# Kernel optimization log

Measured on AMD Instinct MI355X. Metric: run time of the kernel, lower is better.

## Reference

```python
import jax, jax.numpy as jnp
import numpy as np

D_MODEL = 1024
NUM_HEADS = 8
HEAD_DIM = D_MODEL // NUM_HEADS  # 128


def setup_inputs() -> dict:
    key = jax.random.key(0)
    ks = jax.random.split(key, 11)
    B, S = 2, 2048
    inp = {
        "query": jax.random.normal(ks[0], (B, S, D_MODEL), dtype=jnp.float32),
        "key": jax.random.normal(ks[1], (B, S, D_MODEL), dtype=jnp.float32),
        "value": jax.random.normal(ks[2], (B, S, D_MODEL), dtype=jnp.float32),
        # Dense layer params (Keras Dense: y = x @ W + b), glorot-ish scale
        "Wq": jax.random.normal(ks[3], (D_MODEL, D_MODEL), dtype=jnp.float32) * (1.0 / np.sqrt(D_MODEL)),
        "bq": jnp.zeros((D_MODEL,), dtype=jnp.float32),
        "Wk": jax.random.normal(ks[4], (D_MODEL, D_MODEL), dtype=jnp.float32) * (1.0 / np.sqrt(D_MODEL)),
        "bk": jnp.zeros((D_MODEL,), dtype=jnp.float32),
        "Wv": jax.random.normal(ks[5], (D_MODEL, D_MODEL), dtype=jnp.float32) * (1.0 / np.sqrt(D_MODEL)),
        "bv": jnp.zeros((D_MODEL,), dtype=jnp.float32),
        "Wo": jax.random.normal(ks[6], (D_MODEL, D_MODEL), dtype=jnp.float32) * (1.0 / np.sqrt(D_MODEL)),
        "bo": jnp.zeros((D_MODEL,), dtype=jnp.float32),
    }
    return inp


def _split_heads(x, B):
    # [B, S, D] -> [B, H, S, Hd]
    S = x.shape[1]
    return x.reshape(B, S, NUM_HEADS, HEAD_DIM).transpose(0, 2, 1, 3)


def reference(query, key, value, Wq, bq, Wk, bk, Wv, bv, Wo, bo):
    B, S, _ = query.shape
    q = _split_heads(query @ Wq + bq, B)   # [B,H,S,Hd]
    k = _split_heads(key @ Wk + bk, B)
    v = _split_heads(value @ Wv + bv, B)
    # ReLU (non-softmax) attention; scale by sqrt(per-head dk)
    scale = 1.0 / jnp.sqrt(jnp.float32(HEAD_DIM))
    score = jnp.einsum("bhqd,bhkd->bhqk", q, k) * scale  # [B,H,S,S]
    attn_weights = jax.nn.relu(score)
    # dropout inactive at inference (training=None)
    context = jnp.einsum("bhqk,bhkd->bhqd", attn_weights, v)  # [B,H,S,Hd]
    context = context.transpose(0, 2, 1, 3).reshape(B, S, D_MODEL)
    output = context @ Wo + bo
    return (output, attn_weights)
```

## Files before the change

### kernel.cpp

```cpp
#include <hip/hip_runtime.h>
#include <hip/hip_bf16.h>
#include <stdint.h>

#define D_MODEL 1024
#define NHEAD 8
#define HDIM 128
#define BATCH 2
#define SEQ 2048
#define MTOT (BATCH*SEQ)
#define KVBLK 64
#define NT (SEQ/KVBLK)

typedef __attribute__((ext_vector_type(4))) float f32x4;
typedef __attribute__((ext_vector_type(8))) short bf16x8;

__device__ __forceinline__ uint32_t swz128(uint32_t row, uint32_t cb) {
  return row * 128u + (cb ^ ((row & 7u) << 4));
}
__device__ __forceinline__ uint32_t swz256(uint32_t row, uint32_t cb) {
  return row * 256u + (cb ^ ((row & 7u) << 4));
}

__device__ __forceinline__ void gload16(void* lds, const void* g) {
  __builtin_amdgcn_global_load_lds(
      reinterpret_cast<const __attribute__((address_space(1))) uint32_t*>(
          reinterpret_cast<uintptr_t>(g)),
      reinterpret_cast<__attribute__((address_space(3))) uint32_t*>(
          (uint32_t)reinterpret_cast<uintptr_t>(lds)),
      16, 0, 0);
}

__global__ __launch_bounds__(256) void cast3(const float* __restrict__ q,
                                             const float* __restrict__ k,
                                             const float* __restrict__ v,
                                             __hip_bfloat16* __restrict__ out) {
  const float* src = blockIdx.y == 0 ? q : (blockIdx.y == 1 ? k : v);
  const size_t NE = (size_t)MTOT * D_MODEL;
  size_t i = ((size_t)blockIdx.x * 256 + threadIdx.x) * 8;
  float4 a = *reinterpret_cast<const float4*>(src + i);
  float4 b = *reinterpret_cast<const float4*>(src + i + 4);
  __hip_bfloat16 o[8] = {__float2bfloat16(a.x), __float2bfloat16(a.y),
                         __float2bfloat16(a.z), __float2bfloat16(a.w),
                         __float2bfloat16(b.x), __float2bfloat16(b.y),
                         __float2bfloat16(b.z), __float2bfloat16(b.w)};
  *reinterpret_cast<uint4*>(out + blockIdx.y * NE + i) =
      *reinterpret_cast<const uint4*>(o);
}

__global__ __launch_bounds__(256)
void transpose4(const float* __restrict__ s0, const float* __restrict__ s1,
                const float* __restrict__ s2, const float* __restrict__ s3,
                __hip_bfloat16* __restrict__ d0, __hip_bfloat16* __restrict__ d1,
                __hip_bfloat16* __restrict__ d2, __hip_bfloat16* __restrict__ d3) {
  const float* W = blockIdx.z == 0 ? s0 : blockIdx.z == 1 ? s1 : blockIdx.z == 2 ? s2 : s3;
  __hip_bfloat16* Wt = blockIdx.z == 0 ? d0 : blockIdx.z == 1 ? d1 : blockIdx.z == 2 ? d2 : d3;
  __shared__ float t[32][33];
  const int x = threadIdx.x, y = threadIdx.y;
  const int n0 = blockIdx.x * 32, k0 = blockIdx.y * 32;
#pragma unroll
  for (int i = 0; i < 4; ++i)
    t[y + i * 8][x] = W[(size_t)(k0 + y + i * 8) * D_MODEL + n0 + x];
  __syncthreads();
#pragma unroll
  for (int i = 0; i < 4; ++i)
    Wt[(size_t)(n0 + y + i * 8) * D_MODEL + k0 + x] = __float2bfloat16(t[x][y + i * 8]);
}

struct GemmArgs {
  const __hip_bfloat16* A;
  const __hip_bfloat16* B;
  const float* bias;
  void* out;
  int mode;
};

__global__ __launch_bounds__(256)
void gemm_gl(GemmArgs g0, GemmArgs g1, GemmArgs g2, int K) {
  __shared__ char ldsA[128 * 128];
  __shared__ char ldsB[128 * 128];
  GemmArgs ga = blockIdx.z == 0 ? g0 : (blockIdx.z == 1 ? g1 : g2);

  const int tid = threadIdx.x, lane = tid & 63, wid = tid >> 6;
  const int lrow = lane & 15, lko = (lane >> 4) * 8, rbase = (lane >> 4) * 4;
  const int m0 = blockIdx.x * 128, n0 = blockIdx.y * 128;
  const size_t ldb = (size_t)K * 2;

  const int srow = lane >> 3;
  const int sca = ((lane & 7) * 16) ^ (srow << 4);
  const char* Ab = (const char*)ga.A + (size_t)(m0 + wid * 32 + srow) * ldb + sca;
  const char* Bb = (const char*)ga.B + (size_t)(n0 + wid * 32 + srow) * ldb + sca;
  char* lA = ldsA + wid * 32 * 128;
  char* lB = ldsB + wid * 32 * 128;

  f32x4 acc[4][4];
  const f32x4 fz = {0.f, 0.f, 0.f, 0.f};
#pragma unroll
  for (int m = 0; m < 4; ++m)
#pragma unroll
    for (int n = 0; n < 4; ++n) acc[m][n] = fz;

  const int wm = (wid >> 1) * 64, wn = (wid & 1) * 64;

  for (int kt = 0; kt < K; kt += 64) {
    __syncthreads();
#pragma unroll
    for (int i = 0; i < 4; ++i) {
      gload16(lA + i * 8 * 128, Ab + (size_t)i * 8 * ldb + kt * 2);
      gload16(lB + i * 8 * 128, Bb + (size_t)i * 8 * ldb + kt * 2);
    }
    __syncthreads();
#pragma unroll
    for (int kk = 0; kk < 64; kk += 32) {
      bf16x8 af[4], bf[4];
#pragma unroll
      for (int m = 0; m < 4; ++m)
        af[m] = *reinterpret_cast<const bf16x8*>(&ldsA[swz128(wm + m * 16 + lrow, (kk + lko) * 2)]);
#pragma unroll
      for (int n = 0; n < 4; ++n)
        bf[n] = *reinterpret_cast<const bf16x8*>(&ldsB[swz128(wn + n * 16 + lrow, (kk + lko) * 2)]);
#pragma unroll
      for (int m = 0; m < 4; ++m)
#pragma unroll
        for (int n = 0; n < 4; ++n)
          acc[m][n] = __builtin_amdgcn_mfma_f32_16x16x32_bf16(af[m], bf[n], acc[m][n], 0, 0, 0);
    }
  }

  if (ga.mode == 2) {
#pragma unroll
    for (int m = 0; m < 4; ++m)
#pragma unroll
      for (int n = 0; n < 4; ++n) {
        const int col = n0 + wn + n * 16 + lrow;
        const float bv = ga.bias[col];
#pragma unroll
        for (int r = 0; r < 4; ++r) {
          const int row = m0 + wm + m * 16 + rbase + r;
          reinterpret_cast<float*>(ga.out)[(size_t)row * D_MODEL + col] = acc[m][n][r] + bv;
        }
      }
  } else if (ga.mode == 0) {
#pragma unroll
    for (int m = 0; m < 4; ++m)
#pragma unroll
      for (int n = 0; n < 4; ++n) {
        const int col = n0 + wn + n * 16 + lrow;
        const float bv = ga.bias[col];
        const int h = col >> 7, hd = col & 127;
#pragma unroll
        for (int r = 0; r < 4; ++r) {
          const int row = m0 + wm + m * 16 + rbase + r;
          const int b = row >> 11, s = row & 2047;
          reinterpret_cast<__hip_bfloat16*>(ga.out)[((size_t)(b * NHEAD + h) * SEQ + s) * HDIM + hd] =
              __float2bfloat16(acc[m][n][r] + bv);
        }
      }
  } else {
#pragma unroll
    for (int m = 0; m < 4; ++m)
#pragma unroll
      for (int n = 0; n < 4; ++n) {
        const int col = n0 + wn + n * 16 + lrow;
        const float bv = ga.bias[col];
        const int h = col >> 7, hd = col & 127;
#pragma unroll
        for (int r = 0; r < 4; ++r) {
          const int row = m0 + wm + m * 16 + rbase + r;
          const int b = row >> 11, s = row & 2047;
          reinterpret_cast<__hip_bfloat16*>(ga.out)[((size_t)(b * NHEAD + h) * HDIM + hd) * SEQ + s] =
              __float2bfloat16(acc[m][n][r] + bv);
        }
      }
  }
}

__global__ __launch_bounds__(512)
void attn_v2(const __hip_bfloat16* __restrict__ Qh,
             const __hip_bfloat16* __restrict__ Kh,
             const __hip_bfloat16* __restrict__ Vt,
             float* __restrict__ attn,
             __hip_bfloat16* __restrict__ ctx) {
  __shared__ char ldsK[2][KVBLK * 256];
  __shared__ char ldsV[2][HDIM * 128];
  __shared__ char ldsP[128 * 128];

  const int tid = threadIdx.x, lane = tid & 63, wid = tid >> 6;
  const int lrow = lane & 15, lko = (lane >> 4) * 8, rbase = (lane >> 4) * 4;
  const int wqq = (wid >> 1) * 32;
  const int wqk = (wid & 1) * 32;
  const int whd = (wid & 1) * 64;

  const int raw = blockIdx.x;
  const int xcd = raw & 7, slot = raw >> 3;
  const int bh = xcd * 2 + (slot >> 4);
  const int q0 = (slot & 15) * 128;

  const char* Kg = (const char*)Kh + (size_t)bh * SEQ * HDIM * 2;
  const char* Vg = (const char*)Vt + (size_t)bh * HDIM * SEQ * 2;
  const __hip_bfloat16* Qg = Qh + ((size_t)bh * SEQ + q0) * HDIM;
  float* attnb = attn + ((size_t)bh * SEQ + q0) * SEQ;

  const int krl = lane >> 4;
  const int kcb = (lane & 15) * 16;
  const int vrl = lane >> 3;
  const int vsc = ((lane & 7) * 16) ^ (vrl << 4);

#pragma unroll
  for (int j = 0; j < 2; ++j) {
    const int rr = wid * 8 + j * 4 + krl;
    gload16((char*)ldsK[0] + (wid * 8 + j * 4) * 256,
            Kg + (size_t)rr * 256 + (kcb ^ ((rr & 7) << 4)));
    const int rv = wid * 16 + j * 8 + vrl;
    gload16((char*)ldsV[0] + (wid * 16 + j * 8) * 128,
            Vg + (size_t)rv * (SEQ * 2) + vsc);
  }

  bf16x8 qf[2][4];
#pragma unroll
  for (int m = 0; m < 2; ++m)
#pragma unroll
    for (int kk = 0; kk < 4; ++kk)
      qf[m][kk] = *reinterpret_cast<const bf16x8*>(
          Qg + (size_t)(wqq + m * 16 + lrow) * HDIM + kk * 32 + lko);

  f32x4 cacc[2][4];
  const f32x4 fz = {0.f, 0.f, 0.f, 0.f};
#pragma unroll
  for (int m = 0; m < 2; ++m)
#pragma unroll
    for (int n = 0; n < 4; ++n) cacc[m][n] = fz;

  const float scale = 0.08838834764831845f;
  __syncthreads();

  for (int t = 0; t < NT; ++t) {
    const int b = t & 1;
    if (t + 1 < NT) {
#pragma unroll
      for (int j = 0; j < 2; ++j) {
        const int rr = wid * 8 + j * 4 + krl;
        gload16((char*)ldsK[b ^ 1] + (wid * 8 + j * 4) * 256,
                Kg + (size_t)((t + 1) * KVBLK + rr) * 256 + (kcb ^ ((rr & 7) << 4)));
        const int rv = wid * 16 + j * 8 + vrl;
        gload16((char*)ldsV[b ^ 1] + (wid * 16 + j * 8) * 128,
                Vg + (size_t)rv * (SEQ * 2) + (t + 1) * 128 + vsc);
      }
    }

    f32x4 sacc[2][2];
#pragma unroll
    for (int m = 0; m < 2; ++m)
#pragma unroll
      for (int n = 0; n < 2; ++n) sacc[m][n] = fz;
    __builtin_amdgcn_s_setprio(1);
#pragma unroll
    for (int kk = 0; kk < 4; ++kk) {
      bf16x8 kf[2];
#pragma unroll
      for (int n = 0; n < 2; ++n)
        kf[n] = *reinterpret_cast<const bf16x8*>(
            &ldsK[b][swz256(wqk + n * 16 + lrow, (kk * 32 + lko) * 2)]);
#pragma unroll
      for (int m = 0; m < 2; ++m)
#pragma unroll
        for (int n = 0; n < 2; ++n)
          sacc[m][n] = __builtin_amdgcn_mfma_f32_16x16x32_bf16(qf[m][kk], kf[n], sacc[m][n], 0, 0, 0);
    }
    __builtin_amdgcn_s_setprio(0);

#pragma unroll
    for (int m = 0; m < 2; ++m)
#pragma unroll
      for (int n = 0; n < 2; ++n)
#pragma unroll
        for (int r = 0; r < 4; ++r) {
          const int ql = wqq + m * 16 + rbase + r;
          const int kl = wqk + n * 16 + lrow;
          const float s = fmaxf(sacc[m][n][r] * scale, 0.f);
          attnb[(size_t)ql * SEQ + t * KVBLK + kl] = s;
          *reinterpret_cast<__hip_bfloat16*>(&ldsP[swz128(ql, kl * 2)]) = __float2bfloat16(s);
        }
    __syncthreads();

    __builtin_amdgcn_s_setprio(1);
#pragma unroll
    for (int kk = 0; kk < 2; ++kk) {
      bf16x8 pf[2], vf[4];
#pragma unroll
      for (int m = 0; m < 2; ++m)
        pf[m] = *reinterpret_cast<const bf16x8*>(
            &ldsP[swz128(wqq + m * 16 + lrow, (kk * 32 + lko) * 2)]);
#pragma unroll
      for (int n = 0; n < 4; ++n)
        vf[n] = *reinterpret_cast<const bf16x8*>(
            &ldsV[b][swz128(whd + n * 16 + lrow, (kk * 32 + lko) * 2)]);
#pragma unroll
      for (int m = 0; m < 2; ++m)
#pragma unroll
        for (int n = 0; n < 4; ++n)
          cacc[m][n] = __builtin_amdgcn_mfma_f32_16x16x32_bf16(pf[m], vf[n], cacc[m][n], 0, 0, 0);
    }
    __builtin_amdgcn_s_setprio(0);
    __syncthreads();
  }

  const int bb = bh >> 3, h = bh & 7;
#pragma unroll
  for (int m = 0; m < 2; ++m)
#pragma unroll
    for (int n = 0; n < 4; ++n)
#pragma unroll
      for (int r = 0; r < 4; ++r) {
        const int srow = q0 + wqq + m * 16 + rbase + r;
        const int hd = whd + n * 16 + lrow;
        ctx[((size_t)(bb * SEQ + srow)) * D_MODEL + h * HDIM + hd] =
            __float2bfloat16(cacc[m][n][r]);
      }
}

extern "C" void kernel_launch(void* const* d_in, const int* in_sizes, int n_in,
                              void* d_out, int out_size, void* d_ws, size_t ws_size,
                              hipStream_t stream) {
  const float* q  = (const float*)d_in[0];
  const float* k  = (const float*)d_in[1];
  const float* v  = (const float*)d_in[2];
  const float* Wq = (const float*)d_in[3];
  const float* bq = (const float*)d_in[4];
  const float* Wk = (const float*)d_in[5];
  const float* bk = (const float*)d_in[6];
  const float* Wv = (const float*)d_in[7];
  const float* bv = (const float*)d_in[8];
  const float* Wo = (const float*)d_in[9];
  const float* bo = (const float*)d_in[10];

  char* ws = (char*)d_ws;
  const size_t NE = (size_t)MTOT * D_MODEL;
  const size_t WE = (size_t)D_MODEL * D_MODEL;
  __hip_bfloat16* qb  = (__hip_bfloat16*)ws;
  __hip_bfloat16* kb  = qb + NE;
  __hip_bfloat16* vb  = kb + NE;
  __hip_bfloat16* Wqt = vb + NE;
  __hip_bfloat16* Wkt = Wqt + WE;
  __hip_bfloat16* Wvt = Wkt + WE;
  __hip_bfloat16* Wot = Wvt + WE;
  __hip_bfloat16* Qh  = Wot + WE;
  __hip_bfloat16* Kh  = Qh + NE;
  __hip_bfloat16* Vt  = Kh + NE;
  __hip_bfloat16* ctx = Vt + NE;

  cast3<<<dim3((unsigned)(NE / 8 / 256), 3), 256, 0, stream>>>(q, k, v, qb);
  transpose4<<<dim3(32, 32, 4), dim3(32, 8), 0, stream>>>(Wq, Wk, Wv, Wo, Wqt, Wkt, Wvt, Wot);

  GemmArgs gq{qb, Wqt, bq, Qh, 0};
  GemmArgs gk{kb, Wkt, bk, Kh, 0};
  GemmArgs gv{vb, Wvt, bv, Vt, 1};
  gemm_gl<<<dim3(32, 8, 3), 256, 0, stream>>>(gq, gk, gv, D_MODEL);

  float* outp  = (float*)d_out;
  float* attnp = outp + NE;
  attn_v2<<<256, 512, 0, stream>>>(Qh, Kh, Vt, attnp, ctx);

  GemmArgs go{ctx, Wot, bo, d_out, 2};
  gemm_gl<<<dim3(32, 8, 1), 256, 0, stream>>>(go, go, go, D_MODEL);
}
```

Before: 154.9 us.

## Halve attention query tile to 64 rows and double grid size

Shrinks the attention kernel's query block from 128 to 64 rows, so each wave handles 16 query rows instead of 32, and launches 512 blocks instead of 256 with a matching bh/q0 mapping. It also sets a min-blocks occupancy hint and writes the large fp32 attention-weights output with nontemporal stores. The goal is more parallelism and occupancy and less cache pollution from the big score write. In exchange, K/V tiles are loaded from global memory twice as often per query, and each wave issues fewer MFMAs per LDS load.

```diff
diff --git a/kernel.cpp b/kernel.cpp
--- a/kernel.cpp
+++ b/kernel.cpp
@@ -10,6 +10,7 @@
 #define MTOT (BATCH*SEQ)
 #define KVBLK 64
 #define NT (SEQ/KVBLK)
+#define QBLK 64
 
 typedef __attribute__((ext_vector_type(4))) float f32x4;
 typedef __attribute__((ext_vector_type(8))) short bf16x8;
@@ -174,26 +175,25 @@
   }
 }
 
-__global__ __launch_bounds__(512)
-void attn_v2(const __hip_bfloat16* __restrict__ Qh,
+__global__ __launch_bounds__(512, 4)
+void attn_v3(const __hip_bfloat16* __restrict__ Qh,
              const __hip_bfloat16* __restrict__ Kh,
              const __hip_bfloat16* __restrict__ Vt,
              float* __restrict__ attn,
              __hip_bfloat16* __restrict__ ctx) {
   __shared__ char ldsK[2][KVBLK * 256];
   __shared__ char ldsV[2][HDIM * 128];
-  __shared__ char ldsP[128 * 128];
+  __shared__ char ldsP[QBLK * 128];
 
   const int tid = threadIdx.x, lane = tid & 63, wid = tid >> 6;
   const int lrow = lane & 15, lko = (lane >> 4) * 8, rbase = (lane >> 4) * 4;
-  const int wqq = (wid >> 1) * 32;
-  const int wqk = (wid & 1) * 32;
-  const int whd = (wid & 1) * 64;
+  const int qg = (wid >> 1) * 16;
+  const int kg = wid & 1;
 
   const int raw = blockIdx.x;
   const int xcd = raw & 7, slot = raw >> 3;
-  const int bh = xcd * 2 + (slot >> 4);
-  const int q0 = (slot & 15) * 128;
+  const int bh = xcd * 2 + (slot >> 5);
+  const int q0 = (slot & 31) * QBLK;
 
   const char* Kg = (const char*)Kh + (size_t)bh * SEQ * HDIM * 2;
   const char* Vg = (const char*)Vt + (size_t)bh * HDIM * SEQ * 2;
@@ -215,20 +215,16 @@
             Vg + (size_t)rv * (SEQ * 2) + vsc);
   }
 
-  bf16x8 qf[2][4];
-#pragma unroll
-  for (int m = 0; m < 2; ++m)
-#pragma unroll
-    for (int kk = 0; kk < 4; ++kk)
-      qf[m][kk] = *reinterpret_cast<const bf16x8*>(
-          Qg + (size_t)(wqq + m * 16 + lrow) * HDIM + kk * 32 + lko);
-
-  f32x4 cacc[2][4];
+  bf16x8 qf[4];
+#pragma unroll
+  for (int kk = 0; kk < 4; ++kk)
+    qf[kk] = *reinterpret_cast<const bf16x8*>(
+        Qg + (size_t)(qg + lrow) * HDIM + kk * 32 + lko);
+
+  f32x4 cacc[4];
   const f32x4 fz = {0.f, 0.f, 0.f, 0.f};
 #pragma unroll
-  for (int m = 0; m < 2; ++m)
-#pragma unroll
-    for (int n = 0; n < 4; ++n) cacc[m][n] = fz;
+  for (int n = 0; n < 4; ++n) cacc[n] = fz;
 
   const float scale = 0.08838834764831845f;
   __syncthreads();
@@ -247,11 +243,9 @@
       }
     }
 
-    f32x4 sacc[2][2];
-#pragma unroll
-    for (int m = 0; m < 2; ++m)
-#pragma unroll
-      for (int n = 0; n < 2; ++n) sacc[m][n] = fz;
+    f32x4 sacc[2];
+#pragma unroll
+    for (int n = 0; n < 2; ++n) sacc[n] = fz;
     __builtin_amdgcn_s_setprio(1);
 #pragma unroll
     for (int kk = 0; kk < 4; ++kk) {
@@ -259,46 +253,38 @@
 #pragma unroll
       for (int n = 0; n < 2; ++n)
         kf[n] = *reinterpret_cast<const bf16x8*>(
-            &ldsK[b][swz256(wqk + n * 16 + lrow, (kk * 32 + lko) * 2)]);
-#pragma unroll
-      for (int m = 0; m < 2; ++m)
-#pragma unroll
-        for (int n = 0; n < 2; ++n)
-          sacc[m][n] = __builtin_amdgcn_mfma_f32_16x16x32_bf16(qf[m][kk], kf[n], sacc[m][n], 0, 0, 0);
+            &ldsK[b][swz256(kg * 32 + n * 16 + lrow, (kk * 32 + lko) * 2)]);
+#pragma unroll
+      for (int n = 0; n < 2; ++n)
+        sacc[n] = __builtin_amdgcn_mfma_f32_16x16x32_bf16(qf[kk], kf[n], sacc[n], 0, 0, 0);
     }
     __builtin_amdgcn_s_setprio(0);
 
 #pragma unroll
-    for (int m = 0; m < 2; ++m)
-#pragma unroll
-      for (int n = 0; n < 2; ++n)
-#pragma unroll
-        for (int r = 0; r < 4; ++r) {
-          const int ql = wqq + m * 16 + rbase + r;
-          const int kl = wqk + n * 16 + lrow;
-          const float s = fmaxf(sacc[m][n][r] * scale, 0.f);
-          attnb[(size_t)ql * SEQ + t * KVBLK + kl] = s;
-          *reinterpret_cast<__hip_bfloat16*>(&ldsP[swz128(ql, kl * 2)]) = __float2bfloat16(s);
-        }
+    for (int n = 0; n < 2; ++n)
+#pragma unroll
+      for (int r = 0; r < 4; ++r) {
+        const int ql = qg + rbase + r;
+        const int kl = kg * 32 + n * 16 + lrow;
+        const float s = fmaxf(sacc[n][r] * scale, 0.f);
+        __builtin_nontemporal_store(s, &attnb[(size_t)ql * SEQ + t * KVBLK + kl]);
+        *reinterpret_cast<__hip_bfloat16*>(&ldsP[swz128(ql, kl * 2)]) = __float2bfloat16(s);
+      }
     __syncthreads();
 
     __builtin_amdgcn_s_setprio(1);
 #pragma unroll
     for (int kk = 0; kk < 2; ++kk) {
-      bf16x8 pf[2], vf[4];
-#pragma unroll
-      for (int m = 0; m < 2; ++m)
-        pf[m] = *reinterpret_cast<const bf16x8*>(
-            &ldsP[swz128(wqq + m * 16 + lrow, (kk * 32 + lko) * 2)]);
+      bf16x8 pf, vf[4];
+      pf = *reinterpret_cast<const bf16x8*>(
+          &ldsP[swz128(qg + lrow, (kk * 32 + lko) * 2)]);
 #pragma unroll
       for (int n = 0; n < 4; ++n)
         vf[n] = *reinterpret_cast<const bf16x8*>(
-            &ldsV[b][swz128(whd + n * 16 + lrow, (kk * 32 + lko) * 2)]);
-#pragma unroll
-      for (int m = 0; m < 2; ++m)
-#pragma unroll
-        for (int n = 0; n < 4; ++n)
-          cacc[m][n] = __builtin_amdgcn_mfma_f32_16x16x32_bf16(pf[m], vf[n], cacc[m][n], 0, 0, 0);
+            &ldsV[b][swz128(kg * 64 + n * 16 + lrow, (kk * 32 + lko) * 2)]);
+#pragma unroll
+      for (int n = 0; n < 4; ++n)
+        cacc[n] = __builtin_amdgcn_mfma_f32_16x16x32_bf16(pf, vf[n], cacc[n], 0, 0, 0);
     }
     __builtin_amdgcn_s_setprio(0);
     __syncthreads();
@@ -306,16 +292,14 @@
 
   const int bb = bh >> 3, h = bh & 7;
 #pragma unroll
-  for (int m = 0; m < 2; ++m)
-#pragma unroll
-    for (int n = 0; n < 4; ++n)
-#pragma unroll
-      for (int r = 0; r < 4; ++r) {
-        const int srow = q0 + wqq + m * 16 + rbase + r;
-        const int hd = whd + n * 16 + lrow;
-        ctx[((size_t)(bb * SEQ + srow)) * D_MODEL + h * HDIM + hd] =
-            __float2bfloat16(cacc[m][n][r]);
-      }
+  for (int n = 0; n < 4; ++n)
+#pragma unroll
+    for (int r = 0; r < 4; ++r) {
+      const int srow = q0 + qg + rbase + r;
+      const int hd = kg * 64 + n * 16 + lrow;
+      ctx[((size_t)(bb * SEQ + srow)) * D_MODEL + h * HDIM + hd] =
+          __float2bfloat16(cacc[n][r]);
+    }
 }
 
 extern "C" void kernel_launch(void* const* d_in, const int* in_sizes, int n_in,
@@ -358,7 +342,7 @@
 
   float* outp  = (float*)d_out;
   float* attnp = outp + NE;
-  attn_v2<<<256, 512, 0, stream>>>(Qh, Kh, Vt, attnp, ctx);
+  attn_v3<<<512, 512, 0, stream>>>(Qh, Kh, Vt, attnp, ctx);
 
   GemmArgs go{ctx, Wot, bo, d_out, 2};
   gemm_gl<<<dim3(32, 8, 1), 256, 0, stream>>>(go, go, go, D_MODEL);
```

After: 169.0 us. +9.1%, slower.

## Split attention KV range across two blocks and combine partial contexts

Applied to the files above, without the earlier changes.

Doubles the attention grid by splitting each query tile's KV sequence into two halves processed by separate blocks, each writing an fp32 partial context that a new combine kernel sums and casts to bf16. V is now single-buffered and loaded at the start of each iteration, which reduces LDS use so more blocks can be resident (launch bounds request 4). The intent is better CU occupancy on the 256-CU device, at the cost of extra fp32 partial writes, a second kernel launch, and V loads no longer being prefetched a tile ahead.

```diff
diff --git a/kernel.cpp b/kernel.cpp
--- a/kernel.cpp
+++ b/kernel.cpp
@@ -174,14 +174,14 @@
   }
 }
 
-__global__ __launch_bounds__(512)
-void attn_v2(const __hip_bfloat16* __restrict__ Qh,
+__global__ __launch_bounds__(512, 4)
+void attn_v4(const __hip_bfloat16* __restrict__ Qh,
              const __hip_bfloat16* __restrict__ Kh,
              const __hip_bfloat16* __restrict__ Vt,
              float* __restrict__ attn,
-             __hip_bfloat16* __restrict__ ctx) {
+             float* __restrict__ ctxp) {
   __shared__ char ldsK[2][KVBLK * 256];
-  __shared__ char ldsV[2][HDIM * 128];
+  __shared__ char ldsV[HDIM * 128];
   __shared__ char ldsP[128 * 128];
 
   const int tid = threadIdx.x, lane = tid & 63, wid = tid >> 6;
@@ -192,13 +192,17 @@
 
   const int raw = blockIdx.x;
   const int xcd = raw & 7, slot = raw >> 3;
-  const int bh = xcd * 2 + (slot >> 4);
-  const int q0 = (slot & 15) * 128;
+  const int bh = xcd * 2 + (slot >> 5);
+  const int rem = slot & 31;
+  const int part = rem >> 4;
+  const int q0 = (rem & 15) * 128;
+  const int t0 = part * (NT / 2), t1 = t0 + (NT / 2);
 
   const char* Kg = (const char*)Kh + (size_t)bh * SEQ * HDIM * 2;
   const char* Vg = (const char*)Vt + (size_t)bh * HDIM * SEQ * 2;
   const __hip_bfloat16* Qg = Qh + ((size_t)bh * SEQ + q0) * HDIM;
   float* attnb = attn + ((size_t)bh * SEQ + q0) * SEQ;
+  float* ctxb = ctxp + (size_t)part * MTOT * D_MODEL;
 
   const int krl = lane >> 4;
   const int kcb = (lane & 15) * 16;
@@ -209,10 +213,7 @@
   for (int j = 0; j < 2; ++j) {
     const int rr = wid * 8 + j * 4 + krl;
     gload16((char*)ldsK[0] + (wid * 8 + j * 4) * 256,
-            Kg + (size_t)rr * 256 + (kcb ^ ((rr & 7) << 4)));
-    const int rv = wid * 16 + j * 8 + vrl;
-    gload16((char*)ldsV[0] + (wid * 16 + j * 8) * 128,
-            Vg + (size_t)rv * (SEQ * 2) + vsc);
+            Kg + (size_t)(t0 * KVBLK + rr) * 256 + (kcb ^ ((rr & 7) << 4)));
   }
 
   bf16x8 qf[2][4];
@@ -233,17 +234,20 @@
   const float scale = 0.08838834764831845f;
   __syncthreads();
 
-  for (int t = 0; t < NT; ++t) {
+  for (int t = t0; t < t1; ++t) {
     const int b = t & 1;
-    if (t + 1 < NT) {
+#pragma unroll
+    for (int j = 0; j < 2; ++j) {
+      const int rv = wid * 16 + j * 8 + vrl;
+      gload16((char*)ldsV + (wid * 16 + j * 8) * 128,
+              Vg + (size_t)rv * (SEQ * 2) + t * 128 + vsc);
+    }
+    if (t + 1 < t1) {
 #pragma unroll
       for (int j = 0; j < 2; ++j) {
         const int rr = wid * 8 + j * 4 + krl;
         gload16((char*)ldsK[b ^ 1] + (wid * 8 + j * 4) * 256,
                 Kg + (size_t)((t + 1) * KVBLK + rr) * 256 + (kcb ^ ((rr & 7) << 4)));
-        const int rv = wid * 16 + j * 8 + vrl;
-        gload16((char*)ldsV[b ^ 1] + (wid * 16 + j * 8) * 128,
-                Vg + (size_t)rv * (SEQ * 2) + (t + 1) * 128 + vsc);
       }
     }
 
@@ -293,7 +297,7 @@
 #pragma unroll
       for (int n = 0; n < 4; ++n)
         vf[n] = *reinterpret_cast<const bf16x8*>(
-            &ldsV[b][swz128(whd + n * 16 + lrow, (kk * 32 + lko) * 2)]);
+            &ldsV[swz128(whd + n * 16 + lrow, (kk * 32 + lko) * 2)]);
 #pragma unroll
       for (int m = 0; m < 2; ++m)
 #pragma unroll
@@ -313,9 +317,24 @@
       for (int r = 0; r < 4; ++r) {
         const int srow = q0 + wqq + m * 16 + rbase + r;
         const int hd = whd + n * 16 + lrow;
-        ctx[((size_t)(bb * SEQ + srow)) * D_MODEL + h * HDIM + hd] =
-            __float2bfloat16(cacc[m][n][r]);
-      }
+        ctxb[((size_t)(bb * SEQ + srow)) * D_MODEL + h * HDIM + hd] = cacc[m][n][r];
+      }
+}
+
+__global__ __launch_bounds__(256)
+void combine2(const float* __restrict__ p, __hip_bfloat16* __restrict__ ctx) {
+  const size_t NE = (size_t)MTOT * D_MODEL;
+  size_t i = ((size_t)blockIdx.x * 256 + threadIdx.x) * 8;
+  f32x4 a0 = *reinterpret_cast<const f32x4*>(p + i);
+  f32x4 a1 = *reinterpret_cast<const f32x4*>(p + i + 4);
+  f32x4 b0 = *reinterpret_cast<const f32x4*>(p + NE + i);
+  f32x4 b1 = *reinterpret_cast<const f32x4*>(p + NE + i + 4);
+  f32x4 s0 = a0 + b0, s1 = a1 + b1;
+  __hip_bfloat16 o[8] = {__float2bfloat16(s0[0]), __float2bfloat16(s0[1]),
+                         __float2bfloat16(s0[2]), __float2bfloat16(s0[3]),
+                         __float2bfloat16(s1[0]), __float2bfloat16(s1[1]),
+                         __float2bfloat16(s1[2]), __float2bfloat16(s1[3])};
+  *reinterpret_cast<uint4*>(ctx + i) = *reinterpret_cast<const uint4*>(o);
 }
 
 extern "C" void kernel_launch(void* const* d_in, const int* in_sizes, int n_in,
@@ -347,6 +366,7 @@
   __hip_bfloat16* Kh  = Qh + NE;
   __hip_bfloat16* Vt  = Kh + NE;
   __hip_bfloat16* ctx = Vt + NE;
+  float* ctxp = (float*)(ctx + NE);
 
   cast3<<<dim3((unsigned)(NE / 8 / 256), 3), 256, 0, stream>>>(q, k, v, qb);
   transpose4<<<dim3(32, 32, 4), dim3(32, 8), 0, stream>>>(Wq, Wk, Wv, Wo, Wqt, Wkt, Wvt, Wot);
@@ -358,7 +378,8 @@
 
   float* outp  = (float*)d_out;
   float* attnp = outp + NE;
-  attn_v2<<<256, 512, 0, stream>>>(Qh, Kh, Vt, attnp, ctx);
+  attn_v4<<<512, 512, 0, stream>>>(Qh, Kh, Vt, attnp, ctxp);
+  combine2<<<(unsigned)(NE / 8 / 256), 256, 0, stream>>>(ctxp, ctx);
 
   GemmArgs go{ctx, Wot, bo, d_out, 2};
   gemm_gl<<<dim3(32, 8, 1), 256, 0, stream>>>(go, go, go, D_MODEL);
```

Measured after the change: 307.2 us. +98.3%, slower.
